# Optimization experiments

Hardware: AMD Instinct MI355X
Metric: run time of the kernel (lower is better)

The kernel has to match this reference:

```python
import jax, jax.numpy as jnp
import numpy as np

B, S, DM = 4, 2048, 512
H, D = 8, 64          # att_head, head_dim = att_dim // att_head
LEFT, RIGHT = 128, 128  # band_part(left_mask, right_mask)
LARGE = 1e30          # masked_softmax large number for fp32


def setup_inputs() -> dict:
    key = jax.random.key(0)
    ks = jax.random.split(key, 11)
    scale = 1.0 / np.sqrt(DM)
    x = jax.random.normal(ks[0], (B, S, DM), jnp.float32)
    Wq = jax.random.normal(ks[1], (DM, DM), jnp.float32) * scale
    bq = jnp.zeros((DM,), jnp.float32)
    Wk = jax.random.normal(ks[2], (DM, DM), jnp.float32) * scale
    bk = jnp.zeros((DM,), jnp.float32)
    Wv = jax.random.normal(ks[3], (DM, DM), jnp.float32) * scale
    bv = jnp.zeros((DM,), jnp.float32)
    Wo = jax.random.normal(ks[4], (DM, DM), jnp.float32) * scale
    bo = jnp.zeros((DM,), jnp.float32)
    x_len = jax.random.randint(ks[5], (B,), 0, 2048)
    return {"x": x, "Wq": Wq, "bq": bq, "Wk": Wk, "bk": bk,
            "Wv": Wv, "bv": bv, "Wo": Wo, "bo": bo, "x_len": x_len}


def reference(x, Wq, bq, Wk, bk, Wv, bv, Wo, bo, x_len):
    b, s, _ = x.shape
    # QKV projections, split into heads: [B,S,H,D]
    q = (x @ Wq + bq).reshape(b, s, H, D)
    k = (x @ Wk + bk).reshape(b, s, H, D)
    v = (x @ Wv + bv).reshape(b, s, H, D)
    # content energy: [B,H,Q,K], scaled by sqrt(head_dim)
    energy = jnp.einsum('bind,bjnd->bnij', q, k) / jnp.sqrt(jnp.float32(D))
    # banded mask (tf.linalg.band_part semantics): keep -LEFT <= j-i <= RIGHT
    i = jnp.arange(s)[:, None]
    j = jnp.arange(s)[None, :]
    band = ((j - i) <= RIGHT) & ((i - j) <= LEFT)            # [S,S]
    # key-length mask (tf.sequence_mask, expanded to [B,1,1,S])
    seq = jnp.arange(s)[None, :] < x_len[:, None]            # [B,S]
    mask = (band[None, None, :, :] & seq[:, None, None, :]).astype(energy.dtype)
    # masked softmax: energy - (1 - mask) * LARGE, softmax over keys
    att = jax.nn.softmax(energy - (1.0 - mask) * LARGE, axis=-1)
    # context: [B,Q,H,D] -> [B,S,H*D]
    ctx = jnp.einsum('bnij,bjnd->bind', att, v).reshape(b, s, H * D)
    # output projection (use_proj=True)
    return ctx @ Wo + bo
```

## Files before the change

kernel.cpp:

```cpp
#include <hip/hip_runtime.h>

#define S_LEN 2048
#define BATCH 4
#define DMODEL 512
#define NHEAD 8
#define HDIM 64
#define ROWS (BATCH * S_LEN)

using short8 = __attribute__((ext_vector_type(8))) short;
using f32x4  = __attribute__((ext_vector_type(4))) float;

__device__ __forceinline__ unsigned short f2bf(float f) {
  unsigned int u = __builtin_bit_cast(unsigned int, f);
  u += 0x7fffu + ((u >> 16) & 1u);
  return (unsigned short)(u >> 16);
}
__device__ __forceinline__ float bf2f(unsigned short h) {
  unsigned int u = ((unsigned int)h) << 16;
  return __builtin_bit_cast(float, u);
}
__device__ __forceinline__ void glds16(const void* g, void* l) {
  __builtin_amdgcn_global_load_lds((const __attribute__((address_space(1))) unsigned*)g,
                                   (__attribute__((address_space(3))) unsigned*)l, 16, 0, 0);
}

__global__ __launch_bounds__(256) void cvt_bf16_kernel(const float* __restrict__ x,
                                                       unsigned short* __restrict__ xb,
                                                       int n) {
  int t = blockIdx.x * 256 + threadIdx.x;
  int base = t * 8;
  if (base >= n) return;
  float4 f0 = *(const float4*)(x + base);
  float4 f1 = *(const float4*)(x + base + 4);
  uint4 o;
  o.x = (unsigned)f2bf(f0.x) | ((unsigned)f2bf(f0.y) << 16);
  o.y = (unsigned)f2bf(f0.z) | ((unsigned)f2bf(f0.w) << 16);
  o.z = (unsigned)f2bf(f1.x) | ((unsigned)f2bf(f1.y) << 16);
  o.w = (unsigned)f2bf(f1.z) | ((unsigned)f2bf(f1.w) << 16);
  *(uint4*)(xb + base) = o;
}

__global__ void transpose_w_kernel(const float* __restrict__ W,
                                   unsigned short* __restrict__ WT) {
  __shared__ float t[32][33];
  const int tx = threadIdx.x, ty = threadIdx.y;
  const int x0 = blockIdx.x * 32, y0 = blockIdx.y * 32;
#pragma unroll
  for (int r = 0; r < 4; r++)
    t[ty + 8 * r][tx] = W[(size_t)(y0 + ty + 8 * r) * DMODEL + x0 + tx];
  __syncthreads();
#pragma unroll
  for (int r = 0; r < 4; r++)
    WT[(size_t)(x0 + ty + 8 * r) * DMODEL + y0 + tx] = f2bf(t[tx][ty + 8 * r]);
}

template <int MODE>
__global__ __launch_bounds__(256, 2) void gemm128_kernel(const unsigned short* __restrict__ A,
                                                         const unsigned short* __restrict__ Bt,
                                                         const float* __restrict__ bias0,
                                                         const float* __restrict__ bias1,
                                                         void* __restrict__ out0,
                                                         void* __restrict__ out1) {
  constexpr int K = DMODEL;
  __shared__ __align__(16) char smem[16384];
  char* As = smem;
  char* Bs = smem + 8192;
  const int tid = threadIdx.x;
  const int wave = tid >> 6, lane = tid & 63;
  const int wr = wave >> 1, wc = wave & 1;
  const int lm = lane & 15, lq = lane >> 4;
  const int m0 = blockIdx.y * 128, n0 = blockIdx.x * 128;
  const int lr = lane >> 2;
  const int lc = (lane & 3) ^ ((lane >> 3) & 3);
  const unsigned short* gA0 = A + (size_t)(m0 + wave * 16 + lr) * K + lc * 8;
  const unsigned short* gA1 = A + (size_t)(m0 + (wave + 4) * 16 + lr) * K + lc * 8;
  const unsigned short* gB0 = Bt + (size_t)(n0 + wave * 16 + lr) * K + lc * 8;
  const unsigned short* gB1 = Bt + (size_t)(n0 + (wave + 4) * 16 + lr) * K + lc * 8;
  char* lA0 = As + wave * 1024 + lane * 16;
  char* lA1 = As + (wave + 4) * 1024 + lane * 16;
  char* lB0 = Bs + wave * 1024 + lane * 16;
  char* lB1 = Bs + (wave + 4) * 1024 + lane * 16;
  const int sw = (lm >> 1) & 3;
  int aoff[4], boff[4];
#pragma unroll
  for (int mi = 0; mi < 4; mi++)
    aoff[mi] = (wr * 64 + mi * 16 + lm) * 64 + (lq ^ sw) * 16;
#pragma unroll
  for (int ni = 0; ni < 4; ni++)
    boff[ni] = (wc * 64 + ni * 16 + lm) * 64 + (lq ^ sw) * 16;

  f32x4 acc[4][4] = {};
  for (int k0 = 0; k0 < K; k0 += 32) {
    __syncthreads();
    glds16(gA0 + k0, lA0);
    glds16(gA1 + k0, lA1);
    glds16(gB0 + k0, lB0);
    glds16(gB1 + k0, lB1);
    __syncthreads();
    short8 af[4], bfr[4];
#pragma unroll
    for (int mi = 0; mi < 4; mi++) af[mi] = *(const short8*)(As + aoff[mi]);
#pragma unroll
    for (int ni = 0; ni < 4; ni++) bfr[ni] = *(const short8*)(Bs + boff[ni]);
#pragma unroll
    for (int mi = 0; mi < 4; mi++)
#pragma unroll
      for (int ni = 0; ni < 4; ni++)
        acc[mi][ni] = __builtin_amdgcn_mfma_f32_16x16x32_bf16(af[mi], bfr[ni], acc[mi][ni], 0, 0, 0);
  }
#pragma unroll
  for (int mi = 0; mi < 4; mi++) {
    const int row0 = m0 + wr * 64 + mi * 16 + lq * 4;
#pragma unroll
    for (int ni = 0; ni < 4; ni++) {
      const int col = n0 + wc * 64 + ni * 16 + lm;
#pragma unroll
      for (int r = 0; r < 4; r++) {
        const int row = row0 + r;
        const float v = acc[mi][ni][r];
        if (MODE == 0) {
          if (col < DMODEL)
            ((unsigned short*)out0)[(size_t)row * DMODEL + col] = f2bf(v + bias0[col]);
          else
            ((unsigned short*)out1)[(size_t)row * DMODEL + (col - DMODEL)] =
                f2bf(v + bias1[col - DMODEL]);
        } else if (MODE == 1) {
          ((unsigned short*)out0)[(size_t)row * ROWS + col] = f2bf(v + bias0[row]);
        } else {
          ((float*)out0)[(size_t)row * DMODEL + col] = v + bias0[col];
        }
      }
    }
  }
}

__global__ __launch_bounds__(256) void vsum_kernel(const unsigned short* __restrict__ Vt,
                                                   float* __restrict__ vs) {
  const int wid = blockIdx.x * 4 + (threadIdx.x >> 6);
  const int lane = threadIdx.x & 63;
  const int b = wid >> 9, n = wid & 511;
  const unsigned short* row = Vt + (size_t)n * ROWS + b * S_LEN;
  float s = 0.f;
#pragma unroll
  for (int it = 0; it < 4; it++) {
    uint4 v = *(const uint4*)(row + it * 512 + lane * 8);
    unsigned int w[4] = {v.x, v.y, v.z, v.w};
#pragma unroll
    for (int e = 0; e < 4; e++) {
      s += bf2f((unsigned short)(w[e] & 0xffffu));
      s += bf2f((unsigned short)(w[e] >> 16));
    }
  }
#pragma unroll
  for (int off = 1; off < 64; off <<= 1) s += __shfl_xor(s, off, 64);
  if (lane == 0) vs[(size_t)b * DMODEL + n] = s;
}

__global__ __launch_bounds__(256) void attn_kernel(const unsigned short* __restrict__ Q,
                                                   const unsigned short* __restrict__ K,
                                                   const unsigned short* __restrict__ Vt,
                                                   const int* __restrict__ x_len,
                                                   const float* __restrict__ vsum,
                                                   unsigned short* __restrict__ ctx) {
  __shared__ unsigned short Ks[32][72];
  __shared__ unsigned short Vs[64][40];
  __shared__ unsigned short Ps[4][16][40];
  const int tid = threadIdx.x;
  const int wave = tid >> 6, lane = tid & 63;
  const int lm = lane & 15, lq = lane >> 4;
  const int b = blockIdx.z, h = blockIdx.y;
  const int i0 = blockIdx.x * 64;
  const int q0 = i0 + wave * 16;
  const int xlen = x_len[b];

  const size_t qoff = (size_t)(b * S_LEN + q0 + lm) * DMODEL + h * HDIM + lq * 8;
  const short8 aq0 = *(const short8*)(Q + qoff);
  const short8 aq1 = *(const short8*)(Q + qoff + 32);

  const int krow = tid >> 3, kchk = (tid & 7) * 8;
  const int vdim = tid >> 2, vchk = (tid & 3) * 8;

  f32x4 oacc[4] = {};
  float mrow[4] = {-1e30f, -1e30f, -1e30f, -1e30f};
  float lrow[4] = {0.f, 0.f, 0.f, 0.f};

  for (int kt = 0; kt < 10; kt++) {
    const int jt0 = i0 - 128 + kt * 32;
    if (jt0 + 31 < 0 || jt0 >= xlen) continue;
    __syncthreads();
    {
      const int jr = jt0 + krow;
      const int jrc = min(max(jr, 0), S_LEN - 1);
      *(uint4*)&Ks[krow][kchk] =
          *(const uint4*)(K + (size_t)(b * S_LEN + jrc) * DMODEL + h * HDIM + kchk);
      const int jv = jt0 + vchk;
      const int jvc = min(max(jv, 0), S_LEN - 8);
      *(uint4*)&Vs[vdim][vchk] =
          *(const uint4*)(Vt + (size_t)(h * HDIM + vdim) * ROWS + b * S_LEN + jvc);
    }
    __syncthreads();
    if (jt0 + 31 < q0 - 128 || jt0 > q0 + 143) continue;

    f32x4 sv[2];
#pragma unroll
    for (int sub = 0; sub < 2; sub++) {
      const short8 bk0 = *(const short8*)&Ks[sub * 16 + lm][lq * 8];
      const short8 bk1 = *(const short8*)&Ks[sub * 16 + lm][32 + lq * 8];
      f32x4 s = {};
      s = __builtin_amdgcn_mfma_f32_16x16x32_bf16(aq0, bk0, s, 0, 0, 0);
      s = __builtin_amdgcn_mfma_f32_16x16x32_bf16(aq1, bk1, s, 0, 0, 0);
      sv[sub] = s;
    }
#pragma unroll
    for (int sub = 0; sub < 2; sub++) {
      const int j = jt0 + sub * 16 + lm;
      const bool jv = (j >= 0) && (j < xlen);
#pragma unroll
      for (int r = 0; r < 4; r++) {
        const int i = q0 + lq * 4 + r;
        const bool ok = jv && (j - i <= 128) && (i - j <= 128);
        sv[sub][r] = ok ? sv[sub][r] * 0.125f : -1e30f;
      }
    }
    float alpha[4], p0[4], p1[4];
#pragma unroll
    for (int r = 0; r < 4; r++) {
      float mx = fmaxf(sv[0][r], sv[1][r]);
#pragma unroll
      for (int off = 1; off < 16; off <<= 1) mx = fmaxf(mx, __shfl_xor(mx, off, 64));
      const float mn = fmaxf(mrow[r], mx);
      alpha[r] = __expf(mrow[r] - mn);
      mrow[r] = mn;
      p0[r] = (sv[0][r] > -1e29f) ? __expf(sv[0][r] - mn) : 0.f;
      p1[r] = (sv[1][r] > -1e29f) ? __expf(sv[1][r] - mn) : 0.f;
      float rs = p0[r] + p1[r];
#pragma unroll
      for (int off = 1; off < 16; off <<= 1) rs += __shfl_xor(rs, off, 64);
      lrow[r] = lrow[r] * alpha[r] + rs;
    }
#pragma unroll
    for (int r = 0; r < 4; r++) {
      Ps[wave][lq * 4 + r][lm] = f2bf(p0[r]);
      Ps[wave][lq * 4 + r][16 + lm] = f2bf(p1[r]);
    }
    const short8 pf = *(const short8*)&Ps[wave][lm][lq * 8];
#pragma unroll
    for (int dt = 0; dt < 4; dt++) {
#pragma unroll
      for (int r = 0; r < 4; r++) oacc[dt][r] *= alpha[r];
      const short8 bv = *(const short8*)&Vs[dt * 16 + lm][lq * 8];
      oacc[dt] = __builtin_amdgcn_mfma_f32_16x16x32_bf16(pf, bv, oacc[dt], 0, 0, 0);
    }
  }
#pragma unroll
  for (int r = 0; r < 4; r++) {
    const int i = q0 + lq * 4 + r;
    const size_t obase = (size_t)(b * S_LEN + i) * DMODEL + h * HDIM;
    if (lrow[r] > 0.f) {
      const float inv = 1.f / lrow[r];
#pragma unroll
      for (int dt = 0; dt < 4; dt++)
        ctx[obase + dt * 16 + lm] = f2bf(oacc[dt][r] * inv);
    } else {
#pragma unroll
      for (int dt = 0; dt < 4; dt++)
        ctx[obase + dt * 16 + lm] =
            f2bf(vsum[(size_t)b * DMODEL + h * HDIM + dt * 16 + lm] * (1.f / 2048.f));
    }
  }
}

extern "C" void kernel_launch(void* const* d_in, const int* in_sizes, int n_in,
                              void* d_out, int out_size, void* d_ws, size_t ws_size,
                              hipStream_t stream) {
  (void)in_sizes; (void)n_in; (void)out_size; (void)ws_size;
  const float* x  = (const float*)d_in[0];
  const float* Wq = (const float*)d_in[1];
  const float* bq = (const float*)d_in[2];
  const float* Wk = (const float*)d_in[3];
  const float* bk = (const float*)d_in[4];
  const float* Wv = (const float*)d_in[5];
  const float* bv = (const float*)d_in[6];
  const float* Wo = (const float*)d_in[7];
  const float* bo = (const float*)d_in[8];
  const int* x_len = (const int*)d_in[9];

  char* ws = (char*)d_ws;
  const size_t MB = 1024 * 1024;
  unsigned short* xb   = (unsigned short*)(ws + 0 * MB);
  unsigned short* Qb   = (unsigned short*)(ws + 8 * MB);
  unsigned short* Kb   = (unsigned short*)(ws + 16 * MB);
  unsigned short* Vt   = (unsigned short*)(ws + 24 * MB);
  unsigned short* Cx   = (unsigned short*)(ws + 32 * MB);
  unsigned short* WqkT = (unsigned short*)(ws + 40 * MB);
  unsigned short* WvT  = (unsigned short*)(ws + 41 * MB);
  unsigned short* WoT  = (unsigned short*)(ws + 41 * MB + 512 * 1024);
  float* vsum          = (float*)(ws + 42 * MB);

  cvt_bf16_kernel<<<(ROWS * DMODEL) / 2048, 256, 0, stream>>>(x, xb, ROWS * DMODEL);
  dim3 tb(32, 8), tg(16, 16);
  transpose_w_kernel<<<tg, tb, 0, stream>>>(Wq, WqkT);
  transpose_w_kernel<<<tg, tb, 0, stream>>>(Wk, WqkT + 512 * 512);
  transpose_w_kernel<<<tg, tb, 0, stream>>>(Wv, WvT);
  transpose_w_kernel<<<tg, tb, 0, stream>>>(Wo, WoT);

  gemm128_kernel<0><<<dim3(8, 64), 256, 0, stream>>>(xb, WqkT, bq, bk, Qb, Kb);
  gemm128_kernel<1><<<dim3(64, 4), 256, 0, stream>>>(WvT, xb, bv, nullptr, Vt, nullptr);
  vsum_kernel<<<512, 256, 0, stream>>>(Vt, vsum);
  attn_kernel<<<dim3(32, 8, 4), 256, 0, stream>>>(Qb, Kb, Vt, x_len, vsum, Cx);
  gemm128_kernel<2><<<dim3(4, 64), 256, 0, stream>>>(Cx, WoT, bo, nullptr, (float*)d_out, nullptr);
}
```

Measured before the change: 168.0 us.

## Merge prep and QKV launches, skip masked Q/K tiles, widen attention query tile

```diff
diff --git a/kernel.cpp b/kernel.cpp
--- a/kernel.cpp
+++ b/kernel.cpp
@@ -24,27 +24,37 @@
                                    (__attribute__((address_space(3))) unsigned*)l, 16, 0, 0);
 }
 
-__global__ __launch_bounds__(256) void cvt_bf16_kernel(const float* __restrict__ x,
-                                                       unsigned short* __restrict__ xb,
-                                                       int n) {
-  int t = blockIdx.x * 256 + threadIdx.x;
-  int base = t * 8;
-  if (base >= n) return;
-  float4 f0 = *(const float4*)(x + base);
-  float4 f1 = *(const float4*)(x + base + 4);
-  uint4 o;
-  o.x = (unsigned)f2bf(f0.x) | ((unsigned)f2bf(f0.y) << 16);
-  o.y = (unsigned)f2bf(f0.z) | ((unsigned)f2bf(f0.w) << 16);
-  o.z = (unsigned)f2bf(f1.x) | ((unsigned)f2bf(f1.y) << 16);
-  o.w = (unsigned)f2bf(f1.z) | ((unsigned)f2bf(f1.w) << 16);
-  *(uint4*)(xb + base) = o;
-}
-
-__global__ void transpose_w_kernel(const float* __restrict__ W,
-                                   unsigned short* __restrict__ WT) {
+__global__ __launch_bounds__(256) void prep_kernel(const float* __restrict__ x,
+                                                   const float* __restrict__ Wq,
+                                                   const float* __restrict__ Wk,
+                                                   const float* __restrict__ Wv,
+                                                   const float* __restrict__ Wo,
+                                                   unsigned short* __restrict__ xb,
+                                                   unsigned short* __restrict__ WqkT,
+                                                   unsigned short* __restrict__ WvT,
+                                                   unsigned short* __restrict__ WoT) {
   __shared__ float t[32][33];
-  const int tx = threadIdx.x, ty = threadIdx.y;
-  const int x0 = blockIdx.x * 32, y0 = blockIdx.y * 32;
+  const int blk = blockIdx.x, tid = threadIdx.x;
+  if (blk < 2048) {
+    const int base = (blk * 256 + tid) * 8;
+    float4 f0 = *(const float4*)(x + base);
+    float4 f1 = *(const float4*)(x + base + 4);
+    uint4 o;
+    o.x = (unsigned)f2bf(f0.x) | ((unsigned)f2bf(f0.y) << 16);
+    o.y = (unsigned)f2bf(f0.z) | ((unsigned)f2bf(f0.w) << 16);
+    o.z = (unsigned)f2bf(f1.x) | ((unsigned)f2bf(f1.y) << 16);
+    o.w = (unsigned)f2bf(f1.z) | ((unsigned)f2bf(f1.w) << 16);
+    *(uint4*)(xb + base) = o;
+    return;
+  }
+  const int tb = blk - 2048;
+  const int which = tb >> 8;
+  const int tile = tb & 255;
+  const float* W = which == 0 ? Wq : which == 1 ? Wk : which == 2 ? Wv : Wo;
+  unsigned short* WT = which == 0 ? WqkT : which == 1 ? (WqkT + 512 * 512)
+                      : which == 2 ? WvT : WoT;
+  const int tx = tid & 31, ty = tid >> 5;
+  const int x0 = (tile & 15) * 32, y0 = (tile >> 4) * 32;
 #pragma unroll
   for (int r = 0; r < 4; r++)
     t[ty + 8 * r][tx] = W[(size_t)(y0 + ty + 8 * r) * DMODEL + x0 + tx];
@@ -54,13 +64,106 @@
     WT[(size_t)(x0 + ty + 8 * r) * DMODEL + y0 + tx] = f2bf(t[tx][ty + 8 * r]);
 }
 
-template <int MODE>
-__global__ __launch_bounds__(256, 2) void gemm128_kernel(const unsigned short* __restrict__ A,
-                                                         const unsigned short* __restrict__ Bt,
-                                                         const float* __restrict__ bias0,
-                                                         const float* __restrict__ bias1,
-                                                         void* __restrict__ out0,
-                                                         void* __restrict__ out1) {
+__global__ __launch_bounds__(256, 2) void gemm_qkv_kernel(const unsigned short* __restrict__ xb,
+                                                          const unsigned short* __restrict__ WqkT,
+                                                          const unsigned short* __restrict__ WvT,
+                                                          const float* __restrict__ bq,
+                                                          const float* __restrict__ bk,
+                                                          const float* __restrict__ bv,
+                                                          const int* __restrict__ x_len,
+                                                          unsigned short* __restrict__ Qb,
+                                                          unsigned short* __restrict__ Kb,
+                                                          unsigned short* __restrict__ Vt) {
+  constexpr int K = DMODEL;
+  __shared__ __align__(16) char smem[16384];
+  char* As = smem;
+  char* Bs = smem + 8192;
+  const int bid = blockIdx.x;
+  const bool vmode = bid < 256;
+  const unsigned short *A, *Bt;
+  int m0, n0;
+  if (vmode) {
+    m0 = (bid & 3) * 128;
+    n0 = (bid >> 2) * 128;
+    A = WvT; Bt = xb;
+  } else {
+    const int q = bid - 256;
+    m0 = (q >> 3) * 128;
+    n0 = (q & 7) * 128;
+    A = xb; Bt = WqkT;
+    const int xl = x_len[m0 >> 11];
+    const int s0 = m0 & 2047;
+    if (n0 >= DMODEL) { if (s0 >= xl) return; }
+    else if (s0 >= xl + 128) return;
+  }
+  const int tid = threadIdx.x;
+  const int wave = tid >> 6, lane = tid & 63;
+  const int wr = wave >> 1, wc = wave & 1;
+  const int lm = lane & 15, lq = lane >> 4;
+  const int lr = lane >> 2;
+  const int lc = (lane & 3) ^ ((lane >> 3) & 3);
+  const unsigned short* gA0 = A + (size_t)(m0 + wave * 16 + lr) * K + lc * 8;
+  const unsigned short* gA1 = A + (size_t)(m0 + (wave + 4) * 16 + lr) * K + lc * 8;
+  const unsigned short* gB0 = Bt + (size_t)(n0 + wave * 16 + lr) * K + lc * 8;
+  const unsigned short* gB1 = Bt + (size_t)(n0 + (wave + 4) * 16 + lr) * K + lc * 8;
+  char* lA0 = As + wave * 1024 + lane * 16;
+  char* lA1 = As + (wave + 4) * 1024 + lane * 16;
+  char* lB0 = Bs + wave * 1024 + lane * 16;
+  char* lB1 = Bs + (wave + 4) * 1024 + lane * 16;
+  const int sw = (lm >> 1) & 3;
+  int aoff[4], boff[4];
+#pragma unroll
+  for (int mi = 0; mi < 4; mi++)
+    aoff[mi] = (wr * 64 + mi * 16 + lm) * 64 + (lq ^ sw) * 16;
+#pragma unroll
+  for (int ni = 0; ni < 4; ni++)
+    boff[ni] = (wc * 64 + ni * 16 + lm) * 64 + (lq ^ sw) * 16;
+
+  f32x4 acc[4][4] = {};
+  for (int k0 = 0; k0 < K; k0 += 32) {
+    __syncthreads();
+    glds16(gA0 + k0, lA0);
+    glds16(gA1 + k0, lA1);
+    glds16(gB0 + k0, lB0);
+    glds16(gB1 + k0, lB1);
+    __syncthreads();
+    short8 af[4], bfr[4];
+#pragma unroll
+    for (int mi = 0; mi < 4; mi++) af[mi] = *(const short8*)(As + aoff[mi]);
+#pragma unroll
+    for (int ni = 0; ni < 4; ni++) bfr[ni] = *(const short8*)(Bs + boff[ni]);
+#pragma unroll
+    for (int mi = 0; mi < 4; mi++)
+#pragma unroll
+      for (int ni = 0; ni < 4; ni++)
+        acc[mi][ni] = __builtin_amdgcn_mfma_f32_16x16x32_bf16(af[mi], bfr[ni], acc[mi][ni], 0, 0, 0);
+  }
+#pragma unroll
+  for (int mi = 0; mi < 4; mi++) {
+    const int row0 = m0 + wr * 64 + mi * 16 + lq * 4;
+#pragma unroll
+    for (int ni = 0; ni < 4; ni++) {
+      const int col = n0 + wc * 64 + ni * 16 + lm;
+#pragma unroll
+      for (int r = 0; r < 4; r++) {
+        const int row = row0 + r;
+        const float v = acc[mi][ni][r];
+        if (vmode) {
+          Vt[(size_t)row * ROWS + col] = f2bf(v + bv[row]);
+        } else if (col < DMODEL) {
+          Qb[(size_t)row * DMODEL + col] = f2bf(v + bq[col]);
+        } else {
+          Kb[(size_t)row * DMODEL + (col - DMODEL)] = f2bf(v + bk[col - DMODEL]);
+        }
+      }
+    }
+  }
+}
+
+__global__ __launch_bounds__(256, 2) void gemm_out_kernel(const unsigned short* __restrict__ A,
+                                                          const unsigned short* __restrict__ Bt,
+                                                          const float* __restrict__ bias,
+                                                          float* __restrict__ out) {
   constexpr int K = DMODEL;
   __shared__ __align__(16) char smem[16384];
   char* As = smem;
@@ -115,21 +218,8 @@
     for (int ni = 0; ni < 4; ni++) {
       const int col = n0 + wc * 64 + ni * 16 + lm;
 #pragma unroll
-      for (int r = 0; r < 4; r++) {
-        const int row = row0 + r;
-        const float v = acc[mi][ni][r];
-        if (MODE == 0) {
-          if (col < DMODEL)
-            ((unsigned short*)out0)[(size_t)row * DMODEL + col] = f2bf(v + bias0[col]);
-          else
-            ((unsigned short*)out1)[(size_t)row * DMODEL + (col - DMODEL)] =
-                f2bf(v + bias1[col - DMODEL]);
-        } else if (MODE == 1) {
-          ((unsigned short*)out0)[(size_t)row * ROWS + col] = f2bf(v + bias0[row]);
-        } else {
-          ((float*)out0)[(size_t)row * DMODEL + col] = v + bias0[col];
-        }
-      }
+      for (int r = 0; r < 4; r++)
+        out[(size_t)(row0 + r) * DMODEL + col] = acc[mi][ni][r] + bias[col];
     }
   }
 }
@@ -164,27 +254,34 @@
                                                    unsigned short* __restrict__ ctx) {
   __shared__ unsigned short Ks[32][72];
   __shared__ unsigned short Vs[64][40];
-  __shared__ unsigned short Ps[4][16][40];
+  __shared__ unsigned short Ps[4][2][16][40];
   const int tid = threadIdx.x;
   const int wave = tid >> 6, lane = tid & 63;
   const int lm = lane & 15, lq = lane >> 4;
   const int b = blockIdx.z, h = blockIdx.y;
-  const int i0 = blockIdx.x * 64;
-  const int q0 = i0 + wave * 16;
+  const int i0 = blockIdx.x * 128;
+  const int qbase = i0 + wave * 32;
   const int xlen = x_len[b];
 
-  const size_t qoff = (size_t)(b * S_LEN + q0 + lm) * DMODEL + h * HDIM + lq * 8;
-  const short8 aq0 = *(const short8*)(Q + qoff);
-  const short8 aq1 = *(const short8*)(Q + qoff + 32);
+  short8 aq[2][2];
+#pragma unroll
+  for (int g = 0; g < 2; g++) {
+    const size_t qoff = (size_t)(b * S_LEN + qbase + g * 16 + lm) * DMODEL + h * HDIM + lq * 8;
+    aq[g][0] = *(const short8*)(Q + qoff);
+    aq[g][1] = *(const short8*)(Q + qoff + 32);
+  }
 
   const int krow = tid >> 3, kchk = (tid & 7) * 8;
   const int vdim = tid >> 2, vchk = (tid & 3) * 8;
 
-  f32x4 oacc[4] = {};
-  float mrow[4] = {-1e30f, -1e30f, -1e30f, -1e30f};
-  float lrow[4] = {0.f, 0.f, 0.f, 0.f};
-
-  for (int kt = 0; kt < 10; kt++) {
+  f32x4 oacc[2][4] = {};
+  float mrow[2][4], lrow[2][4];
+#pragma unroll
+  for (int g = 0; g < 2; g++)
+#pragma unroll
+    for (int r = 0; r < 4; r++) { mrow[g][r] = -1e30f; lrow[g][r] = 0.f; }
+
+  for (int kt = 0; kt < 12; kt++) {
     const int jt0 = i0 - 128 + kt * 32;
     if (jt0 + 31 < 0 || jt0 >= xlen) continue;
     __syncthreads();
@@ -199,75 +296,82 @@
           *(const uint4*)(Vt + (size_t)(h * HDIM + vdim) * ROWS + b * S_LEN + jvc);
     }
     __syncthreads();
-    if (jt0 + 31 < q0 - 128 || jt0 > q0 + 143) continue;
-
-    f32x4 sv[2];
-#pragma unroll
-    for (int sub = 0; sub < 2; sub++) {
-      const short8 bk0 = *(const short8*)&Ks[sub * 16 + lm][lq * 8];
-      const short8 bk1 = *(const short8*)&Ks[sub * 16 + lm][32 + lq * 8];
-      f32x4 s = {};
-      s = __builtin_amdgcn_mfma_f32_16x16x32_bf16(aq0, bk0, s, 0, 0, 0);
-      s = __builtin_amdgcn_mfma_f32_16x16x32_bf16(aq1, bk1, s, 0, 0, 0);
-      sv[sub] = s;
-    }
-#pragma unroll
-    for (int sub = 0; sub < 2; sub++) {
-      const int j = jt0 + sub * 16 + lm;
-      const bool jv = (j >= 0) && (j < xlen);
+    if (jt0 + 159 < qbase || jt0 > qbase + 159) continue;
+
+#pragma unroll
+    for (int g = 0; g < 2; g++) {
+      const int qg = qbase + g * 16;
+      if (jt0 + 31 < qg - 128 || jt0 > qg + 143) continue;
+      f32x4 sv[2];
+#pragma unroll
+      for (int sub = 0; sub < 2; sub++) {
+        const short8 bk0 = *(const short8*)&Ks[sub * 16 + lm][lq * 8];
+        const short8 bk1 = *(const short8*)&Ks[sub * 16 + lm][32 + lq * 8];
+        f32x4 s = {};
+        s = __builtin_amdgcn_mfma_f32_16x16x32_bf16(aq[g][0], bk0, s, 0, 0, 0);
+        s = __builtin_amdgcn_mfma_f32_16x16x32_bf16(aq[g][1], bk1, s, 0, 0, 0);
+        sv[sub] = s;
+      }
+#pragma unroll
+      for (int sub = 0; sub < 2; sub++) {
+        const int j = jt0 + sub * 16 + lm;
+        const bool jv = (j >= 0) && (j < xlen);
+#pragma unroll
+        for (int r = 0; r < 4; r++) {
+          const int i = qg + lq * 4 + r;
+          const bool ok = jv && (j - i <= 128) && (i - j <= 128);
+          sv[sub][r] = ok ? sv[sub][r] * 0.125f : -1e30f;
+        }
+      }
+      float alpha[4], p0[4], p1[4];
 #pragma unroll
       for (int r = 0; r < 4; r++) {
-        const int i = q0 + lq * 4 + r;
-        const bool ok = jv && (j - i <= 128) && (i - j <= 128);
-        sv[sub][r] = ok ? sv[sub][r] * 0.125f : -1e30f;
-      }
-    }
-    float alpha[4], p0[4], p1[4];
+        float mx = fmaxf(sv[0][r], sv[1][r]);
+#pragma unroll
+        for (int off = 1; off < 16; off <<= 1) mx = fmaxf(mx, __shfl_xor(mx, off, 64));
+        const float mn = fmaxf(mrow[g][r], mx);
+        alpha[r] = __expf(mrow[g][r] - mn);
+        mrow[g][r] = mn;
+        p0[r] = (sv[0][r] > -1e29f) ? __expf(sv[0][r] - mn) : 0.f;
+        p1[r] = (sv[1][r] > -1e29f) ? __expf(sv[1][r] - mn) : 0.f;
+        float rs = p0[r] + p1[r];
+#pragma unroll
+        for (int off = 1; off < 16; off <<= 1) rs += __shfl_xor(rs, off, 64);
+        lrow[g][r] = lrow[g][r] * alpha[r] + rs;
+      }
+#pragma unroll
+      for (int r = 0; r < 4; r++) {
+        Ps[wave][g][lq * 4 + r][lm] = f2bf(p0[r]);
+        Ps[wave][g][lq * 4 + r][16 + lm] = f2bf(p1[r]);
+      }
+      const short8 pf = *(const short8*)&Ps[wave][g][lm][lq * 8];
+#pragma unroll
+      for (int dt = 0; dt < 4; dt++) {
+#pragma unroll
+        for (int r = 0; r < 4; r++) oacc[g][dt][r] *= alpha[r];
+        const short8 bv = *(const short8*)&Vs[dt * 16 + lm][lq * 8];
+        oacc[g][dt] = __builtin_amdgcn_mfma_f32_16x16x32_bf16(pf, bv, oacc[g][dt], 0, 0, 0);
+      }
+    }
+  }
+#pragma unroll
+  for (int g = 0; g < 2; g++)
 #pragma unroll
     for (int r = 0; r < 4; r++) {
-      float mx = fmaxf(sv[0][r], sv[1][r]);
-#pragma unroll
-      for (int off = 1; off < 16; off <<= 1) mx = fmaxf(mx, __shfl_xor(mx, off, 64));
-      const float mn = fmaxf(mrow[r], mx);
-      alpha[r] = __expf(mrow[r] - mn);
-      mrow[r] = mn;
-      p0[r] = (sv[0][r] > -1e29f) ? __expf(sv[0][r] - mn) : 0.f;
-      p1[r] = (sv[1][r] > -1e29f) ? __expf(sv[1][r] - mn) : 0.f;
-      float rs = p0[r] + p1[r];
-#pragma unroll
-      for (int off = 1; off < 16; off <<= 1) rs += __shfl_xor(rs, off, 64);
-      lrow[r] = lrow[r] * alpha[r] + rs;
-    }
-#pragma unroll
-    for (int r = 0; r < 4; r++) {
-      Ps[wave][lq * 4 + r][lm] = f2bf(p0[r]);
-      Ps[wave][lq * 4 + r][16 + lm] = f2bf(p1[r]);
-    }
-    const short8 pf = *(const short8*)&Ps[wave][lm][lq * 8];
-#pragma unroll
-    for (int dt = 0; dt < 4; dt++) {
-#pragma unroll
-      for (int r = 0; r < 4; r++) oacc[dt][r] *= alpha[r];
-      const short8 bv = *(const short8*)&Vs[dt * 16 + lm][lq * 8];
-      oacc[dt] = __builtin_amdgcn_mfma_f32_16x16x32_bf16(pf, bv, oacc[dt], 0, 0, 0);
-    }
-  }
-#pragma unroll
-  for (int r = 0; r < 4; r++) {
-    const int i = q0 + lq * 4 + r;
-    const size_t obase = (size_t)(b * S_LEN + i) * DMODEL + h * HDIM;
-    if (lrow[r] > 0.f) {
-      const float inv = 1.f / lrow[r];
-#pragma unroll
-      for (int dt = 0; dt < 4; dt++)
-        ctx[obase + dt * 16 + lm] = f2bf(oacc[dt][r] * inv);
-    } else {
-#pragma unroll
-      for (int dt = 0; dt < 4; dt++)
-        ctx[obase + dt * 16 + lm] =
-            f2bf(vsum[(size_t)b * DMODEL + h * HDIM + dt * 16 + lm] * (1.f / 2048.f));
-    }
-  }
+      const int i = qbase + g * 16 + lq * 4 + r;
+      const size_t obase = (size_t)(b * S_LEN + i) * DMODEL + h * HDIM;
+      if (lrow[g][r] > 0.f) {
+        const float inv = 1.f / lrow[g][r];
+#pragma unroll
+        for (int dt = 0; dt < 4; dt++)
+          ctx[obase + dt * 16 + lm] = f2bf(oacc[g][dt][r] * inv);
+      } else {
+#pragma unroll
+        for (int dt = 0; dt < 4; dt++)
+          ctx[obase + dt * 16 + lm] =
+              f2bf(vsum[(size_t)b * DMODEL + h * HDIM + dt * 16 + lm] * (1.f / 2048.f));
+      }
+    }
 }
 
 extern "C" void kernel_launch(void* const* d_in, const int* in_sizes, int n_in,
@@ -297,16 +401,9 @@
   unsigned short* WoT  = (unsigned short*)(ws + 41 * MB + 512 * 1024);
   float* vsum          = (float*)(ws + 42 * MB);
 
-  cvt_bf16_kernel<<<(ROWS * DMODEL) / 2048, 256, 0, stream>>>(x, xb, ROWS * DMODEL);
-  dim3 tb(32, 8), tg(16, 16);
-  transpose_w_kernel<<<tg, tb, 0, stream>>>(Wq, WqkT);
-  transpose_w_kernel<<<tg, tb, 0, stream>>>(Wk, WqkT + 512 * 512);
-  transpose_w_kernel<<<tg, tb, 0, stream>>>(Wv, WvT);
-  transpose_w_kernel<<<tg, tb, 0, stream>>>(Wo, WoT);
-
-  gemm128_kernel<0><<<dim3(8, 64), 256, 0, stream>>>(xb, WqkT, bq, bk, Qb, Kb);
-  gemm128_kernel<1><<<dim3(64, 4), 256, 0, stream>>>(WvT, xb, bv, nullptr, Vt, nullptr);
+  prep_kernel<<<3072, 256, 0, stream>>>(x, Wq, Wk, Wv, Wo, xb, WqkT, WvT, WoT);
+  gemm_qkv_kernel<<<768, 256, 0, stream>>>(xb, WqkT, WvT, bq, bk, bv, x_len, Qb, Kb, Vt);
   vsum_kernel<<<512, 256, 0, stream>>>(Vt, vsum);
-  attn_kernel<<<dim3(32, 8, 4), 256, 0, stream>>>(Qb, Kb, Vt, x_len, vsum, Cx);
-  gemm128_kernel<2><<<dim3(4, 64), 256, 0, stream>>>(Cx, WoT, bo, nullptr, (float*)d_out, nullptr);
-}
+  attn_kernel<<<dim3(16, 8, 4), 256, 0, stream>>>(Qb, Kb, Vt, x_len, vsum, Cx);
+  gemm_out_kernel<<<dim3(4, 64), 256, 0, stream>>>(Cx, WoT, bo, (float*)d_out);
+}
```

Result: no change. 170.8 us (+1.6%).
